# Kernel tuning notes

Measured on AMD Instinct MI355X. Metric: run time of the kernel, lower is better.

The kernel has to match this reference:

```python
import jax, jax.numpy as jnp
import numpy as np

OUT_F, IN_F = 4096, 4096
N_CLUSTERS = 256
B, S = 4, 2048


def setup_inputs() -> dict:
    key = jax.random.key(0)
    k1, k2, k3 = jax.random.split(key, 3)
    input_ = jax.random.normal(k1, (B, S, IN_F), dtype=jnp.float32)
    # centroid table: [n_clusters, 1] (embedding_dim = 1, scalar centroids)
    centroid_table = jax.random.normal(k2, (N_CLUSTERS, 1), dtype=jnp.float32) * 0.02
    # per-element centroid indices for the weight matrix [out_features, in_features]
    weight_idx = jax.random.randint(k3, (OUT_F, IN_F), 0, N_CLUSTERS, dtype=jnp.int32)
    return {"input_": input_, "centroid_table": centroid_table, "weight_idx": weight_idx}


def reference(input_, centroid_table, weight_idx):
    # Dequantize: gather scalar centroid per weight element -> [out_f, in_f]
    weights = centroid_table[:, 0][weight_idx]
    # F.linear(x, W): out = x @ W.T -> [B, S, out_f]
    out = jnp.einsum('bsi,oi->bso', input_, weights)
    return out
```

## Files before the change

### kernel.cpp

```cpp
#include <hip/hip_runtime.h>

typedef unsigned short u16;
typedef __attribute__((ext_vector_type(8))) __bf16 bf16x8;
typedef __attribute__((ext_vector_type(4))) float f32x4;
typedef __attribute__((ext_vector_type(4))) int i32x4;
typedef __attribute__((ext_vector_type(8))) unsigned short u16x8;

#define IN_F 4096
#define OUT_F 4096
#define MDIM 8192

__device__ __forceinline__ u16 f2bf(float f) {
  union { float f; unsigned int u; } v; v.f = f;
  unsigned int r = (v.u + 0x7fffu + ((v.u >> 16) & 1u)) >> 16;
  return (u16)r;
}

#define DQ_BLOCKS (OUT_F * IN_F / (8 * 256))
#define CV_BLOCKS (MDIM * IN_F / (8 * 256))

__global__ __launch_bounds__(256) void prep_kernel(const int* __restrict__ idx,
                                                   const float* __restrict__ table,
                                                   const float* __restrict__ X,
                                                   u16* __restrict__ Wb,
                                                   u16* __restrict__ Xb) {
  int b = blockIdx.x;
  if (b < DQ_BLOCKS) {
    __shared__ float cent[256];
    cent[threadIdx.x] = table[threadIdx.x];
    __syncthreads();
    size_t i = (size_t)b * 256 + threadIdx.x;
    const i32x4* p = (const i32x4*)idx + 2 * i;
    i32x4 v0 = __builtin_nontemporal_load(p);
    i32x4 v1 = __builtin_nontemporal_load(p + 1);
    u16x8 o;
    o[0] = f2bf(cent[v0[0]]); o[1] = f2bf(cent[v0[1]]);
    o[2] = f2bf(cent[v0[2]]); o[3] = f2bf(cent[v0[3]]);
    o[4] = f2bf(cent[v1[0]]); o[5] = f2bf(cent[v1[1]]);
    o[6] = f2bf(cent[v1[2]]); o[7] = f2bf(cent[v1[3]]);
    ((u16x8*)Wb)[i] = o;
  } else {
    size_t i = (size_t)(b - DQ_BLOCKS) * 256 + threadIdx.x;
    const f32x4* p = (const f32x4*)X + 2 * i;
    f32x4 v0 = __builtin_nontemporal_load(p);
    f32x4 v1 = __builtin_nontemporal_load(p + 1);
    u16x8 o;
    o[0] = f2bf(v0[0]); o[1] = f2bf(v0[1]); o[2] = f2bf(v0[2]); o[3] = f2bf(v0[3]);
    o[4] = f2bf(v1[0]); o[5] = f2bf(v1[1]); o[6] = f2bf(v1[2]); o[7] = f2bf(v1[3]);
    ((u16x8*)Xb)[i] = o;
  }
}

#define BM 256
#define BN 256
#define BK 64
#define NKT (IN_F / BK)

__device__ __forceinline__ void gld_lds16(const u16* g, u16* l) {
  __builtin_amdgcn_global_load_lds((const __attribute__((address_space(1))) void*)g,
                                   (__attribute__((address_space(3))) void*)l,
                                   16, 0, 0);
}

#define SBAR   __builtin_amdgcn_s_barrier()
#define VMCNT6 asm volatile("s_waitcnt vmcnt(6)" ::: "memory")
#define VMCNT0 asm volatile("s_waitcnt vmcnt(0)" ::: "memory")

#define STAGE2(SRC, DSTBASE)                                   \
  { const u16* _g = (SRC); u16* _l = (DSTBASE) + sdst;         \
    gld_lds16(_g, _l);                                         \
    gld_lds16(_g + 32, _l + 4096); }

#define LOAD_A(AF, HOFF)                                                   \
  _Pragma("unroll")                                                        \
  for (int mj = 0; mj < 4; ++mj) {                                         \
    AF[mj][0] = *(const bf16x8*)(Ac + (HOFF) + a_row + mj * 512 + s0);     \
    AF[mj][1] = *(const bf16x8*)(Ac + (HOFF) + a_row + mj * 512 + 4096 + s0); \
  }

#define LOAD_B(BF, HOFF)                                                   \
  _Pragma("unroll")                                                        \
  for (int nj = 0; nj < 2; ++nj) {                                         \
    BF[nj][0] = *(const bf16x8*)(Bc + (HOFF) + b_row + nj * 512 + s0);     \
    BF[nj][1] = *(const bf16x8*)(Bc + (HOFF) + b_row + nj * 512 + 4096 + s0); \
  }

#define MFMA_QUAD(AF, BF, MO, NO)                                          \
  _Pragma("unroll")                                                        \
  for (int mj = 0; mj < 4; ++mj) {                                         \
    _Pragma("unroll")                                                      \
    for (int nj = 0; nj < 2; ++nj) {                                       \
      acc[(MO) + mj][(NO) + nj] = __builtin_amdgcn_mfma_f32_16x16x32_bf16( \
          AF[mj][0], BF[nj][0], acc[(MO) + mj][(NO) + nj], 0, 0, 0);       \
      acc[(MO) + mj][(NO) + nj] = __builtin_amdgcn_mfma_f32_16x16x32_bf16( \
          AF[mj][1], BF[nj][1], acc[(MO) + mj][(NO) + nj], 0, 0, 0);       \
    }                                                                      \
  }

__global__ __launch_bounds__(512, 2) void gemm_kernel(const u16* __restrict__ Xb,
                                                      const u16* __restrict__ Wb,
                                                      float* __restrict__ out) {
  __shared__ __align__(16) u16 As[2][2 * 128 * BK];
  __shared__ __align__(16) u16 Bs[2][2 * 128 * BK];

  const int tid = threadIdx.x;
  const int lane = tid & 63;
  const int wv = tid >> 6;
  const int wm_i = wv >> 2;
  const int wn_i = wv & 3;

  const int orig = blockIdx.x;
  const int wgid = (orig & 7) * 64 + (orig >> 3);
  const int bm = wgid >> 4;
  const int bn = wgid & 15;

  const int srow = (tid >> 6) * 16 + (lane >> 2);
  const int c0 = ((lane & 3) - ((lane >> 3) & 3)) & 3;
  const size_t stg_off = (size_t)srow * IN_F + (size_t)c0 * 8;
  const u16* Ag = Xb + (size_t)bm * BM * IN_F + stg_off;
  const u16* Bg = Wb + (size_t)bn * BN * IN_F + stg_off;
  const int sdst = wv * 512;

  const int l15 = lane & 15;
  const int h4 = lane >> 4;
  const int s0 = ((h4 + (l15 >> 1)) & 3) * 8;
  const int a_row = (wm_i * 64 + l15) * 32;
  const int b_row = (wn_i * 32 + l15) * 32;

  f32x4 acc[8][4] = {};
  bf16x8 a[4][2], b0[2][2], b1[2][2];

  STAGE2(Ag, (u16*)As[0]);
  STAGE2(Bg, (u16*)Bs[0]);
  STAGE2(Bg + (size_t)128 * IN_F, (u16*)Bs[0] + 8192);
  STAGE2(Ag + (size_t)128 * IN_F, (u16*)As[0] + 8192);
  STAGE2(Ag + BK, (u16*)As[1]);
  STAGE2(Bg + BK, (u16*)Bs[1]);
  STAGE2(Bg + (size_t)128 * IN_F + BK, (u16*)Bs[1] + 8192);
  VMCNT6;
  SBAR;

  for (int kt = 0; kt < NKT; ++kt) {
    const u16* Ac = As[kt & 1];
    const u16* Bc = Bs[kt & 1];
    u16* Ab = (u16*)As[kt & 1];
    u16* An = (u16*)As[(kt + 1) & 1];
    u16* Bb = (u16*)Bs[kt & 1];
    const size_t k1 = (size_t)((kt + 1 < NKT) ? kt + 1 : NKT - 1) * BK;
    const size_t k2 = (size_t)((kt + 2 < NKT) ? kt + 2 : NKT - 1) * BK;

    LOAD_A(a, 0);
    LOAD_B(b0, 0);
    STAGE2(Ag + (size_t)128 * IN_F + k1, An + 8192);
    SBAR;
    __builtin_amdgcn_s_setprio(1);
    MFMA_QUAD(a, b0, 0, 0);
    __builtin_amdgcn_s_setprio(0);

    LOAD_B(b1, 8192);
    SBAR;
    __builtin_amdgcn_s_setprio(1);
    MFMA_QUAD(a, b1, 0, 2);
    __builtin_amdgcn_s_setprio(0);

    LOAD_A(a, 8192);
    STAGE2(Ag + k2, Ab);
    SBAR;
    __builtin_amdgcn_s_setprio(1);
    MFMA_QUAD(a, b1, 4, 2);
    __builtin_amdgcn_s_setprio(0);

    STAGE2(Bg + k2, Bb);
    STAGE2(Bg + (size_t)128 * IN_F + k2, Bb + 8192);
    VMCNT6;
    SBAR;
    __builtin_amdgcn_s_setprio(1);
    MFMA_QUAD(a, b0, 4, 0);
    __builtin_amdgcn_s_setprio(0);
  }

  VMCNT0;

  const size_t obase = (size_t)(bm * BM) * OUT_F + (size_t)(bn * BN) + (size_t)(wn_i * 32 + l15);
#pragma unroll
  for (int mi = 0; mi < 8; ++mi) {
    const int row = (mi >> 2) * 128 + wm_i * 64 + (mi & 3) * 16 + h4 * 4;
#pragma unroll
    for (int r = 0; r < 4; ++r) {
      float* op = out + obase + (size_t)(row + r) * OUT_F;
#pragma unroll
      for (int ni = 0; ni < 4; ++ni)
        __builtin_nontemporal_store(acc[mi][ni][r], op + (ni >> 1) * 128 + (ni & 1) * 16);
    }
  }
}

extern "C" void kernel_launch(void* const* d_in, const int* in_sizes, int n_in,
                              void* d_out, int out_size, void* d_ws, size_t ws_size,
                              hipStream_t stream) {
  const float* X = (const float*)d_in[0];
  const float* table = (const float*)d_in[1];
  const int* idx = (const int*)d_in[2];
  float* out = (float*)d_out;

  u16* Wb = (u16*)d_ws;
  u16* Xb = Wb + (size_t)OUT_F * IN_F;

  prep_kernel<<<DQ_BLOCKS + CV_BLOCKS, 256, 0, stream>>>(idx, table, X, Wb, Xb);
  gemm_kernel<<<(MDIM / BM) * (OUT_F / BN), 512, 0, stream>>>(Xb, Wb, out);
}
```

Baseline: 476.4 us.

## Restructure GEMM prefetch to one-tile lookahead and grid-stride the prep kernel

```diff
diff --git a/kernel.cpp b/kernel.cpp
--- a/kernel.cpp
+++ b/kernel.cpp
@@ -4,50 +4,43 @@
 typedef __attribute__((ext_vector_type(8))) __bf16 bf16x8;
 typedef __attribute__((ext_vector_type(4))) float f32x4;
 typedef __attribute__((ext_vector_type(4))) int i32x4;
-typedef __attribute__((ext_vector_type(8))) unsigned short u16x8;
+typedef __attribute__((ext_vector_type(4))) unsigned short u16x4;
 
 #define IN_F 4096
 #define OUT_F 4096
 #define MDIM 8192
 
-__device__ __forceinline__ u16 f2bf(float f) {
-  union { float f; unsigned int u; } v; v.f = f;
-  unsigned int r = (v.u + 0x7fffu + ((v.u >> 16) & 1u)) >> 16;
-  return (u16)r;
+__device__ __forceinline__ u16 bfc(float f) {
+  union { __bf16 h; u16 u; } c; c.h = (__bf16)f; return c.u;
 }
 
-#define DQ_BLOCKS (OUT_F * IN_F / (8 * 256))
-#define CV_BLOCKS (MDIM * IN_F / (8 * 256))
+#define PREP_BLOCKS 2048
+#define NU_DQ ((unsigned)(OUT_F) * (unsigned)(IN_F) / 4u)
+#define NU_ALL (NU_DQ + (unsigned)(MDIM) * (unsigned)(IN_F) / 4u)
 
 __global__ __launch_bounds__(256) void prep_kernel(const int* __restrict__ idx,
                                                    const float* __restrict__ table,
                                                    const float* __restrict__ X,
                                                    u16* __restrict__ Wb,
                                                    u16* __restrict__ Xb) {
-  int b = blockIdx.x;
-  if (b < DQ_BLOCKS) {
-    __shared__ float cent[256];
-    cent[threadIdx.x] = table[threadIdx.x];
-    __syncthreads();
-    size_t i = (size_t)b * 256 + threadIdx.x;
-    const i32x4* p = (const i32x4*)idx + 2 * i;
-    i32x4 v0 = __builtin_nontemporal_load(p);
-    i32x4 v1 = __builtin_nontemporal_load(p + 1);
-    u16x8 o;
-    o[0] = f2bf(cent[v0[0]]); o[1] = f2bf(cent[v0[1]]);
-    o[2] = f2bf(cent[v0[2]]); o[3] = f2bf(cent[v0[3]]);
-    o[4] = f2bf(cent[v1[0]]); o[5] = f2bf(cent[v1[1]]);
-    o[6] = f2bf(cent[v1[2]]); o[7] = f2bf(cent[v1[3]]);
-    ((u16x8*)Wb)[i] = o;
-  } else {
-    size_t i = (size_t)(b - DQ_BLOCKS) * 256 + threadIdx.x;
-    const f32x4* p = (const f32x4*)X + 2 * i;
-    f32x4 v0 = __builtin_nontemporal_load(p);
-    f32x4 v1 = __builtin_nontemporal_load(p + 1);
-    u16x8 o;
-    o[0] = f2bf(v0[0]); o[1] = f2bf(v0[1]); o[2] = f2bf(v0[2]); o[3] = f2bf(v0[3]);
-    o[4] = f2bf(v1[0]); o[5] = f2bf(v1[1]); o[6] = f2bf(v1[2]); o[7] = f2bf(v1[3]);
-    ((u16x8*)Xb)[i] = o;
+  __shared__ float cent[256];
+  cent[threadIdx.x] = table[threadIdx.x];
+  __syncthreads();
+  const unsigned stride = PREP_BLOCKS * 256u;
+  for (unsigned u = blockIdx.x * 256u + threadIdx.x; u < NU_ALL; u += stride) {
+    if (u < NU_DQ) {
+      i32x4 v = __builtin_nontemporal_load((const i32x4*)idx + u);
+      u16x4 o;
+      o[0] = bfc(cent[v[0]]); o[1] = bfc(cent[v[1]]);
+      o[2] = bfc(cent[v[2]]); o[3] = bfc(cent[v[3]]);
+      ((u16x4*)Wb)[u] = o;
+    } else {
+      unsigned uc = u - NU_DQ;
+      f32x4 v = __builtin_nontemporal_load((const f32x4*)X + uc);
+      u16x4 o;
+      o[0] = bfc(v[0]); o[1] = bfc(v[1]); o[2] = bfc(v[2]); o[3] = bfc(v[3]);
+      ((u16x4*)Xb)[uc] = o;
+    }
   }
 }
 
@@ -64,6 +57,7 @@
 
 #define SBAR   __builtin_amdgcn_s_barrier()
 #define VMCNT6 asm volatile("s_waitcnt vmcnt(6)" ::: "memory")
+#define VMCNT2 asm volatile("s_waitcnt vmcnt(2)" ::: "memory")
 #define VMCNT0 asm volatile("s_waitcnt vmcnt(0)" ::: "memory")
 
 #define STAGE2(SRC, DSTBASE)                                   \
@@ -134,47 +128,35 @@
   STAGE2(Bg, (u16*)Bs[0]);
   STAGE2(Bg + (size_t)128 * IN_F, (u16*)Bs[0] + 8192);
   STAGE2(Ag + (size_t)128 * IN_F, (u16*)As[0] + 8192);
-  STAGE2(Ag + BK, (u16*)As[1]);
-  STAGE2(Bg + BK, (u16*)Bs[1]);
-  STAGE2(Bg + (size_t)128 * IN_F + BK, (u16*)Bs[1] + 8192);
-  VMCNT6;
+  VMCNT2;
   SBAR;
 
   for (int kt = 0; kt < NKT; ++kt) {
     const u16* Ac = As[kt & 1];
     const u16* Bc = Bs[kt & 1];
-    u16* Ab = (u16*)As[kt & 1];
     u16* An = (u16*)As[(kt + 1) & 1];
-    u16* Bb = (u16*)Bs[kt & 1];
+    u16* Bn = (u16*)Bs[(kt + 1) & 1];
     const size_t k1 = (size_t)((kt + 1 < NKT) ? kt + 1 : NKT - 1) * BK;
-    const size_t k2 = (size_t)((kt + 2 < NKT) ? kt + 2 : NKT - 1) * BK;
 
     LOAD_A(a, 0);
     LOAD_B(b0, 0);
-    STAGE2(Ag + (size_t)128 * IN_F + k1, An + 8192);
+    LOAD_B(b1, 8192);
+    STAGE2(Ag + k1, An);
+    STAGE2(Bg + k1, Bn);
+    STAGE2(Bg + (size_t)128 * IN_F + k1, Bn + 8192);
+    VMCNT6;
     SBAR;
     __builtin_amdgcn_s_setprio(1);
     MFMA_QUAD(a, b0, 0, 0);
-    __builtin_amdgcn_s_setprio(0);
-
-    LOAD_B(b1, 8192);
-    SBAR;
-    __builtin_amdgcn_s_setprio(1);
     MFMA_QUAD(a, b1, 0, 2);
     __builtin_amdgcn_s_setprio(0);
 
     LOAD_A(a, 8192);
-    STAGE2(Ag + k2, Ab);
+    STAGE2(Ag + (size_t)128 * IN_F + k1, An + 8192);
+    VMCNT2;
     SBAR;
     __builtin_amdgcn_s_setprio(1);
     MFMA_QUAD(a, b1, 4, 2);
-    __builtin_amdgcn_s_setprio(0);
-
-    STAGE2(Bg + k2, Bb);
-    STAGE2(Bg + (size_t)128 * IN_F + k2, Bb + 8192);
-    VMCNT6;
-    SBAR;
-    __builtin_amdgcn_s_setprio(1);
     MFMA_QUAD(a, b0, 4, 0);
     __builtin_amdgcn_s_setprio(0);
   }
@@ -206,6 +188,6 @@
   u16* Wb = (u16*)d_ws;
   u16* Xb = Wb + (size_t)OUT_F * IN_F;
 
-  prep_kernel<<<DQ_BLOCKS + CV_BLOCKS, 256, 0, stream>>>(idx, table, X, Wb, Xb);
+  prep_kernel<<<PREP_BLOCKS, 256, 0, stream>>>(idx, table, X, Wb, Xb);
   gemm_kernel<<<(MDIM / BM) * (OUT_F / BN), 512, 0, stream>>>(Xb, Wb, out);
 }
```

New measurement: 466.5 us. 1.02x faster.
